# Kernel optimization log

Hardware: AMD Instinct MI355X
Metric: run time of the kernel (lower is better)

## Reference

```python
import jax, jax.numpy as jnp
import numpy as np
import math

B, L, D = 4, 4096, 1024
M = 256  # num random features
EPS = 1e-06


def setup_inputs() -> dict:
    key = jax.random.key(0)
    kq, kk, kv, kp = jax.random.split(key, 4)
    Q = jax.random.normal(kq, (B, L, D), dtype=jnp.float32)
    K = jax.random.normal(kk, (B, L, D), dtype=jnp.float32)
    V = jax.random.normal(kv, (B, L, D), dtype=jnp.float32)
    # Gaussian random projection (ortho_features=False path): shape (num_features, d_model)
    projection = jax.random.normal(kp, (M, D), dtype=jnp.float32)
    return {"Q": Q, "K": K, "V": V, "projection": projection}


def reference(Q, K, V, projection):
    d_model = Q.shape[-1]
    m = projection.shape[0]
    inv_sqrt_d = 1.0 / math.sqrt(d_model)
    # random features: exp((x / sqrt(d)) @ P^T)
    rf_q = jnp.exp(jnp.einsum('bld,md->blm', Q * inv_sqrt_d, projection)) / math.sqrt(m)  # (B,L,M)
    rf_k = jnp.exp(jnp.einsum('bld,md->blm', K * inv_sqrt_d, projection))                 # (B,L,M)
    # linear attention: KV state and normalizer
    KV = jnp.einsum('blm,bld->bmd', rf_k, V)   # (B,M,D)
    Z = jnp.sum(rf_k, axis=1)                   # (B,M)
    out = jnp.einsum('blm,bmd->bld', rf_q, KV)  # (B,L,D)
    normalizer = jnp.einsum('blm,bm->bl', rf_q, Z) + EPS  # (B,L)
    return out / normalizer[..., None]
```

## Files before the change

### kernel.cpp

```cpp
#include <hip/hip_runtime.h>
#include <math.h>

#define NB 4
#define LL 4096
#define DD 1024
#define MM 256

typedef short s16x8 __attribute__((ext_vector_type(8)));
typedef short s16x4 __attribute__((ext_vector_type(4)));
typedef float fx4 __attribute__((ext_vector_type(4)));
typedef unsigned u32x2 __attribute__((ext_vector_type(2)));
typedef unsigned u32x4 __attribute__((ext_vector_type(4)));

__device__ __forceinline__ float b2f(short s) {
  union { unsigned u; float f; } v;
  v.u = ((unsigned)(unsigned short)s) << 16;
  return v.f;
}
__device__ __forceinline__ short f2b(float f) {
  union { float f; unsigned u; } v;
  v.f = f;
  unsigned r = (v.u + 0x7fffu + ((v.u >> 16) & 1u)) >> 16;
  return (short)(unsigned short)r;
}
__device__ __forceinline__ unsigned cvt2(float lo, float hi) {
  unsigned r;
  asm("v_cvt_pk_bf16_f32 %0, %1, %2" : "=v"(r) : "v"(lo), "v"(hi));
  return r;
}
__device__ __forceinline__ int swz(int row, int col) {
  return row * 64 + (col ^ ((row & 7) << 3));
}
__device__ __forceinline__ int keyf(int m) { return (m ^ (m >> 2)) & 3; }

typedef __attribute__((address_space(1))) const void* gas1_t;
typedef __attribute__((address_space(3))) void* las3_t;
#define GLL16(g, l) __builtin_amdgcn_global_load_lds((gas1_t)(const void*)(g), (las3_t)(void*)(l), 16, 0, 0)

__global__ __launch_bounds__(256) void k_cast(const float* __restrict__ in, short* __restrict__ out, int n4) {
  int i = blockIdx.x * 256 + threadIdx.x;
  if (i >= n4) return;
  float4 v = ((const float4*)in)[i];
  s16x4 s;
  s[0] = f2b(v.x); s[1] = f2b(v.y); s[2] = f2b(v.z); s[3] = f2b(v.w);
  ((s16x4*)out)[i] = s;
}

__global__ __launch_bounds__(512, 2) void k_qk(const float* __restrict__ Q, const float* __restrict__ K,
                                               const short* __restrict__ Pb,
                                               short* __restrict__ rfq, short* __restrict__ rfkT,
                                               float* __restrict__ Zz) {
  __shared__ short As[2][8192];
  __shared__ short Bs[2][16384];
  int b = blockIdx.z;
  int l0 = blockIdx.x * 64;
  int phase = (blockIdx.x + blockIdx.z * 4) & 15;
  int tid = threadIdx.x, lane = tid & 63, w = tid >> 6;
  int wr = w >> 2, wq = w & 3;
  int m16 = lane & 15, kg = lane >> 4;

  int arow = tid >> 2, acol = (tid & 3) * 16;
  int akey = (arow & 7) << 3;
  const float* Xr = (arow < 64 ? Q + ((size_t)b * LL + l0 + arow) * DD
                               : K + ((size_t)b * LL + l0 + arow - 64) * DD) + acol;

  fx4 acc[4][4] = {};
  float4 pa[4];

  {
    int d0 = phase * 64;
    #pragma unroll
    for (int i = 0; i < 4; ++i) pa[i] = *(const float4*)(Xr + d0 + i * 4);
    #pragma unroll
    for (int j = 0; j < 4; ++j) {
      int fl = tid + j * 512, row = fl >> 3, c8 = fl & 7;
      GLL16(Pb + (size_t)row * DD + d0 + (c8 ^ (row & 7)) * 8, &Bs[0][fl * 8]);
    }
    u32x4 v0;
    v0[0] = cvt2(pa[0].x, pa[0].y); v0[1] = cvt2(pa[0].z, pa[0].w);
    v0[2] = cvt2(pa[1].x, pa[1].y); v0[3] = cvt2(pa[1].z, pa[1].w);
    *(u32x4*)&As[0][arow * 64 + (acol ^ akey)] = v0;
    v0[0] = cvt2(pa[2].x, pa[2].y); v0[1] = cvt2(pa[2].z, pa[2].w);
    v0[2] = cvt2(pa[3].x, pa[3].y); v0[3] = cvt2(pa[3].z, pa[3].w);
    *(u32x4*)&As[0][arow * 64 + ((acol + 8) ^ akey)] = v0;
  }
  __syncthreads();

  for (int t = 0; t < 16; ++t) {
    int cur = t & 1, nxt = cur ^ 1;
    if (t < 15) {
      int d1 = (((t + 1) + phase) & 15) * 64;
      #pragma unroll
      for (int i = 0; i < 4; ++i) pa[i] = *(const float4*)(Xr + d1 + i * 4);
      #pragma unroll
      for (int j = 0; j < 4; ++j) {
        int fl = tid + j * 512, row = fl >> 3, c8 = fl & 7;
        GLL16(Pb + (size_t)row * DD + d1 + (c8 ^ (row & 7)) * 8, &Bs[nxt][fl * 8]);
      }
    }
    #pragma unroll
    for (int ks = 0; ks < 2; ++ks) {
      int kb = ks * 32 + kg * 8;
      s16x8 af[4], bf[4];
      #pragma unroll
      for (int mi = 0; mi < 4; ++mi) af[mi] = *(const s16x8*)&As[cur][swz(wr * 64 + mi * 16 + m16, kb)];
      #pragma unroll
      for (int ni = 0; ni < 4; ++ni) bf[ni] = *(const s16x8*)&Bs[cur][swz(wq * 64 + ni * 16 + m16, kb)];
      #pragma unroll
      for (int mi = 0; mi < 4; ++mi)
        #pragma unroll
        for (int ni = 0; ni < 4; ++ni)
          acc[mi][ni] = __builtin_amdgcn_mfma_f32_16x16x32_bf16(af[mi], bf[ni], acc[mi][ni], 0, 0, 0);
    }
    if (t < 15) {
      u32x4 v0;
      v0[0] = cvt2(pa[0].x, pa[0].y); v0[1] = cvt2(pa[0].z, pa[0].w);
      v0[2] = cvt2(pa[1].x, pa[1].y); v0[3] = cvt2(pa[1].z, pa[1].w);
      *(u32x4*)&As[nxt][arow * 64 + (acol ^ akey)] = v0;
      v0[0] = cvt2(pa[2].x, pa[2].y); v0[1] = cvt2(pa[2].z, pa[2].w);
      v0[2] = cvt2(pa[3].x, pa[3].y); v0[3] = cvt2(pa[3].z, pa[3].w);
      *(u32x4*)&As[nxt][arow * 64 + ((acol + 8) ^ akey)] = v0;
    }
    __syncthreads();
  }

  if (wr == 0) {
    #pragma unroll
    for (int mi = 0; mi < 4; ++mi)
      #pragma unroll
      for (int ni = 0; ni < 4; ++ni) {
        int r0 = mi * 16 + (kg << 2);
        int c = wq * 64 + ni * 16 + m16;
        #pragma unroll
        for (int u = 0; u < 4; ++u)
          rfq[((size_t)b * LL + l0 + r0 + u) * MM + c] = f2b(expf(acc[mi][ni][u] * 0.03125f) * 0.0625f);
      }
  } else {
    short* T = (short*)Bs;
    float zp[4] = {0.f, 0.f, 0.f, 0.f};
    #pragma unroll
    for (int mi = 0; mi < 4; ++mi)
      #pragma unroll
      for (int ni = 0; ni < 4; ++ni) {
        int l = mi * 16 + (kg << 2);
        int m = wq * 64 + ni * 16 + m16;
        int key = (m & 7) << 3;
        float e0 = expf(acc[mi][ni][0] * 0.03125f);
        float e1 = expf(acc[mi][ni][1] * 0.03125f);
        float e2 = expf(acc[mi][ni][2] * 0.03125f);
        float e3 = expf(acc[mi][ni][3] * 0.03125f);
        zp[ni] += e0 + e1 + e2 + e3;
        *(unsigned*)&T[m * 64 + (l ^ key)] = cvt2(e0, e1);
        *(unsigned*)&T[m * 64 + ((l ^ key) + 2)] = cvt2(e2, e3);
      }
    #pragma unroll
    for (int ni = 0; ni < 4; ++ni) {
      zp[ni] += __shfl_xor(zp[ni], 16);
      zp[ni] += __shfl_xor(zp[ni], 32);
    }
    if (kg == 0) {
      #pragma unroll
      for (int ni = 0; ni < 4; ++ni)
        atomicAdd(&Zz[b * MM + wq * 64 + ni * 16 + m16], zp[ni]);
    }
  }
  __syncthreads();
  if (tid >= 256) {
    int m = tid - 256, mkey = (m & 7) << 3;
    const short* T = (const short*)Bs;
    short* dst = rfkT + ((size_t)b * MM + m) * LL + l0;
    #pragma unroll
    for (int j = 0; j < 8; ++j) {
      s16x8 v = *(const s16x8*)&T[m * 64 + ((j * 8) ^ mkey)];
      *(s16x8*)(dst + j * 8) = v;
    }
  }
}

__global__ __launch_bounds__(512) void k_kv(const float* __restrict__ V, const short* __restrict__ rfkT,
                                            float* __restrict__ KVp) {
  __shared__ float Vs[2][32 * 129];
  __shared__ short Ak[2][256 * 32];
  int d0 = blockIdx.x * 128, kc = blockIdx.y, b = blockIdx.z;
  int ls = kc * 512;
  int tid = threadIdx.x, lane = tid & 63, w = tid >> 6;
  int wm = w >> 1, wd = w & 1;
  int m16 = lane & 15, kg = lane >> 4;

  int vl = tid >> 4, vf = (tid & 15) * 8;
  const float* Vb = V + ((size_t)b * LL + ls + vl) * DD + d0 + vf;

  int am = tid >> 2, as = tid & 3;
  int acs = as ^ keyf(am);
  const short* AkS0 = rfkT + ((size_t)b * MM + am) * LL + ls + acs * 8;
  const short* AkS1 = rfkT + ((size_t)b * MM + am + 128) * LL + ls + acs * 8;

  fx4 acc[4][4] = {};
  float4 pv0, pv1;

  pv0 = *(const float4*)(Vb);
  pv1 = *(const float4*)(Vb + 4);
  GLL16(AkS0, &Ak[0][tid * 8]);
  GLL16(AkS1, &Ak[0][(tid + 512) * 8]);
  #pragma unroll
  for (int j = 0; j < 4; ++j) {
    Vs[0][vl * 129 + vf + j] = ((const float*)&pv0)[j];
    Vs[0][vl * 129 + vf + 4 + j] = ((const float*)&pv1)[j];
  }
  __syncthreads();

  for (int ch = 0; ch < 16; ++ch) {
    int cur = ch & 1, nxt = cur ^ 1;
    if (ch < 15) {
      int lo = (ch + 1) * 32;
      pv0 = *(const float4*)(Vb + (size_t)lo * DD);
      pv1 = *(const float4*)(Vb + (size_t)lo * DD + 4);
      GLL16(AkS0 + lo, &Ak[nxt][tid * 8]);
      GLL16(AkS1 + lo, &Ak[nxt][(tid + 512) * 8]);
    }
    s16x8 af[4];
    #pragma unroll
    for (int mi = 0; mi < 4; ++mi) {
      int m = wm * 64 + mi * 16 + m16;
      af[mi] = *(const s16x8*)&Ak[cur][m * 32 + ((kg ^ keyf(m)) * 8)];
    }
    #pragma unroll
    for (int ni = 0; ni < 4; ++ni) {
      int d = wd * 64 + ni * 16 + m16;
      const float* vs = &Vs[cur][kg * 8 * 129 + d];
      u32x4 bw;
      bw[0] = cvt2(vs[0], vs[129]);
      bw[1] = cvt2(vs[258], vs[387]);
      bw[2] = cvt2(vs[516], vs[645]);
      bw[3] = cvt2(vs[774], vs[903]);
      s16x8 bf = *(s16x8*)&bw;
      #pragma unroll
      for (int mi = 0; mi < 4; ++mi)
        acc[mi][ni] = __builtin_amdgcn_mfma_f32_16x16x32_bf16(af[mi], bf, acc[mi][ni], 0, 0, 0);
    }
    if (ch < 15) {
      #pragma unroll
      for (int j = 0; j < 4; ++j) {
        Vs[nxt][vl * 129 + vf + j] = ((const float*)&pv0)[j];
        Vs[nxt][vl * 129 + vf + 4 + j] = ((const float*)&pv1)[j];
      }
    }
    __syncthreads();
  }

  float* dst = KVp + (((size_t)kc * NB + b) * DD + d0) * MM;
  #pragma unroll
  for (int mi = 0; mi < 4; ++mi)
    #pragma unroll
    for (int ni = 0; ni < 4; ++ni) {
      int d = wd * 64 + ni * 16 + m16;
      int m = wm * 64 + mi * 16 + (kg << 2);
      *(float4*)(dst + (size_t)d * MM + m) = *(float4*)&acc[mi][ni];
    }
}

__global__ __launch_bounds__(256) void k_red(const float* __restrict__ KVp, short* __restrict__ KVTb) {
  int i = blockIdx.x * 256 + threadIdx.x;
  const float4* p = (const float4*)KVp;
  float4 s = p[i];
  #pragma unroll
  for (int k = 1; k < 8; ++k) {
    float4 v = p[i + k * 262144];
    s.x += v.x; s.y += v.y; s.z += v.z; s.w += v.w;
  }
  u32x2 o;
  o[0] = cvt2(s.x, s.y);
  o[1] = cvt2(s.z, s.w);
  ((u32x2*)KVTb)[i] = o;
}

__global__ __launch_bounds__(512) void k_out(const short* __restrict__ rfq, const short* __restrict__ KVTb,
                                             const float* __restrict__ Zz, float* __restrict__ out) {
  __shared__ short Aq[2][8192];
  __shared__ short Bv[2][8192];
  __shared__ float zl[256];
  __shared__ float np[512];
  __shared__ float nf[128];
  int l0 = blockIdx.x * 128, d0 = blockIdx.y * 128, b = blockIdx.z;
  int tid = threadIdx.x, lane = tid & 63, w = tid >> 6;
  int wr = w >> 2, wc = w & 3;
  const short* Ab = rfq + ((size_t)b * LL + l0) * MM;
  const short* Bb = KVTb + ((size_t)b * DD + d0) * MM;
  int f1 = tid + 512;
  int ar0 = tid >> 3, ac0 = tid & 7, ar1 = f1 >> 3, ac1 = f1 & 7;
  int nrow = tid & 127, nsub = tid >> 7;
  if (tid < 256) zl[tid] = Zz[b * MM + tid];
  fx4 acc[4][2] = {};
  float na = 0.f;

  GLL16(Ab + (size_t)ar0 * MM + (ac0 ^ (ar0 & 7)) * 8, &Aq[0][tid * 8]);
  GLL16(Ab + (size_t)ar1 * MM + (ac1 ^ (ar1 & 7)) * 8, &Aq[0][f1 * 8]);
  GLL16(Bb + (size_t)ar0 * MM + (ac0 ^ (ar0 & 7)) * 8, &Bv[0][tid * 8]);
  GLL16(Bb + (size_t)ar1 * MM + (ac1 ^ (ar1 & 7)) * 8, &Bv[0][f1 * 8]);
  __syncthreads();

  for (int t = 0; t < 4; ++t) {
    int cur = t & 1, nxt = cur ^ 1;
    if (t < 3) {
      int m1 = (t + 1) * 64;
      GLL16(Ab + (size_t)ar0 * MM + m1 + (ac0 ^ (ar0 & 7)) * 8, &Aq[nxt][tid * 8]);
      GLL16(Ab + (size_t)ar1 * MM + m1 + (ac1 ^ (ar1 & 7)) * 8, &Aq[nxt][f1 * 8]);
      GLL16(Bb + (size_t)ar0 * MM + m1 + (ac0 ^ (ar0 & 7)) * 8, &Bv[nxt][tid * 8]);
      GLL16(Bb + (size_t)ar1 * MM + m1 + (ac1 ^ (ar1 & 7)) * 8, &Bv[nxt][f1 * 8]);
    }
    #pragma unroll
    for (int kk = 0; kk < 16; ++kk) {
      int k = nsub * 16 + kk;
      na += b2f(Aq[cur][nrow * 64 + (k ^ ((nrow & 7) << 3))]) * zl[t * 64 + k];
    }
    #pragma unroll
    for (int ks = 0; ks < 2; ++ks) {
      int kb = ks * 32 + (lane >> 4) * 8;
      s16x8 af[4], bf[2];
      #pragma unroll
      for (int mi = 0; mi < 4; ++mi) {
        int row = wr * 64 + mi * 16 + (lane & 15);
        af[mi] = *(const s16x8*)&Aq[cur][row * 64 + (kb ^ ((row & 7) << 3))];
      }
      #pragma unroll
      for (int ni = 0; ni < 2; ++ni) {
        int row = wc * 32 + ni * 16 + (lane & 15);
        bf[ni] = *(const s16x8*)&Bv[cur][row * 64 + (kb ^ ((row & 7) << 3))];
      }
      #pragma unroll
      for (int mi = 0; mi < 4; ++mi)
        #pragma unroll
        for (int ni = 0; ni < 2; ++ni)
          acc[mi][ni] = __builtin_amdgcn_mfma_f32_16x16x32_bf16(af[mi], bf[ni], acc[mi][ni], 0, 0, 0);
    }
    __syncthreads();
  }
  np[tid] = na;
  __syncthreads();
  if (tid < 128) nf[tid] = np[tid] + np[tid + 128] + np[tid + 256] + np[tid + 384] + 1e-6f;
  __syncthreads();
  #pragma unroll
  for (int mi = 0; mi < 4; ++mi)
    #pragma unroll
    for (int ni = 0; ni < 2; ++ni) {
      int l = wr * 64 + mi * 16 + ((lane >> 4) << 2);
      int d = d0 + wc * 32 + ni * 16 + (lane & 15);
      #pragma unroll
      for (int u = 0; u < 4; ++u)
        out[((size_t)b * LL + l0 + l + u) * DD + d] = acc[mi][ni][u] / nf[l + u];
    }
}

extern "C" void kernel_launch(void* const* d_in, const int* in_sizes, int n_in,
                              void* d_out, int out_size, void* d_ws, size_t ws_size,
                              hipStream_t stream) {
  const float* Q = (const float*)d_in[0];
  const float* K = (const float*)d_in[1];
  const float* V = (const float*)d_in[2];
  const float* P = (const float*)d_in[3];
  float* out = (float*)d_out;
  char* ws = (char*)d_ws;

  short* Pb   = (short*)(ws + 0);
  float* Zz   = (float*)(ws + 524288);
  short* KVTb = (short*)(ws + 528384);
  short* rfq  = (short*)(ws + 4722688);
  short* rfkT = (short*)(ws + 13111296);
  float* KVp  = (float*)(ws + 21499904);

  k_cast<<<256, 256, 0, stream>>>(P, Pb, 65536);
  (void)hipMemsetAsync(Zz, 0, 4096, stream);
  k_qk<<<dim3(64, 1, NB), 512, 0, stream>>>(Q, K, Pb, rfq, rfkT, Zz);
  k_kv<<<dim3(8, 8, NB), 512, 0, stream>>>(V, rfkT, KVp);
  k_red<<<1024, 256, 0, stream>>>(KVp, KVTb);
  k_out<<<dim3(32, 8, NB), 512, 0, stream>>>(rfq, KVTb, Zz, out);
}
```

Baseline: 124.8 us.

## Fuse KV split reduction into k_kv via last-block counter and widen k_out tiles

Drops the separate k_red launch. Each k_kv block increments a per-slice atomic counter, and the last of the eight L-chunk blocks sums the partial KV slices and writes the bf16 transposed KV. k_out now covers 256 output columns per block (4x4 MFMA tiles per wave), halving the grid and the redundant rfq loads and normalizer work. k_qk also drops the per-block phase rotation of the D loop, so all blocks read the projection in the same order. The trade-offs are a serialized tail reduction in one block per slice, more LDS and registers in k_out, and possible L2 or channel hotspotting without the phase offset.

```diff
diff --git a/kernel.cpp b/kernel.cpp
--- a/kernel.cpp
+++ b/kernel.cpp
@@ -54,7 +54,6 @@
   __shared__ short Bs[2][16384];
   int b = blockIdx.z;
   int l0 = blockIdx.x * 64;
-  int phase = (blockIdx.x + blockIdx.z * 4) & 15;
   int tid = threadIdx.x, lane = tid & 63, w = tid >> 6;
   int wr = w >> 2, wq = w & 3;
   int m16 = lane & 15, kg = lane >> 4;
@@ -67,15 +66,14 @@
   fx4 acc[4][4] = {};
   float4 pa[4];
 
+  #pragma unroll
+  for (int i = 0; i < 4; ++i) pa[i] = *(const float4*)(Xr + i * 4);
+  #pragma unroll
+  for (int j = 0; j < 4; ++j) {
+    int fl = tid + j * 512, row = fl >> 3, c8 = fl & 7;
+    GLL16(Pb + (size_t)row * DD + (c8 ^ (row & 7)) * 8, &Bs[0][fl * 8]);
+  }
   {
-    int d0 = phase * 64;
-    #pragma unroll
-    for (int i = 0; i < 4; ++i) pa[i] = *(const float4*)(Xr + d0 + i * 4);
-    #pragma unroll
-    for (int j = 0; j < 4; ++j) {
-      int fl = tid + j * 512, row = fl >> 3, c8 = fl & 7;
-      GLL16(Pb + (size_t)row * DD + d0 + (c8 ^ (row & 7)) * 8, &Bs[0][fl * 8]);
-    }
     u32x4 v0;
     v0[0] = cvt2(pa[0].x, pa[0].y); v0[1] = cvt2(pa[0].z, pa[0].w);
     v0[2] = cvt2(pa[1].x, pa[1].y); v0[3] = cvt2(pa[1].z, pa[1].w);
@@ -89,7 +87,7 @@
   for (int t = 0; t < 16; ++t) {
     int cur = t & 1, nxt = cur ^ 1;
     if (t < 15) {
-      int d1 = (((t + 1) + phase) & 15) * 64;
+      int d1 = (t + 1) * 64;
       #pragma unroll
       for (int i = 0; i < 4; ++i) pa[i] = *(const float4*)(Xr + d1 + i * 4);
       #pragma unroll
@@ -178,9 +176,11 @@
 }
 
 __global__ __launch_bounds__(512) void k_kv(const float* __restrict__ V, const short* __restrict__ rfkT,
-                                            float* __restrict__ KVp) {
+                                            float* __restrict__ KVp, short* __restrict__ KVTb,
+                                            unsigned* __restrict__ cnt) {
   __shared__ float Vs[2][32 * 129];
   __shared__ short Ak[2][256 * 32];
+  __shared__ unsigned isLast;
   int d0 = blockIdx.x * 128, kc = blockIdx.y, b = blockIdx.z;
   int ls = kc * 512;
   int tid = threadIdx.x, lane = tid & 63, w = tid >> 6;
@@ -257,56 +257,76 @@
       int m = wm * 64 + mi * 16 + (kg << 2);
       *(float4*)(dst + (size_t)d * MM + m) = *(float4*)&acc[mi][ni];
     }
-}
-
-__global__ __launch_bounds__(256) void k_red(const float* __restrict__ KVp, short* __restrict__ KVTb) {
-  int i = blockIdx.x * 256 + threadIdx.x;
-  const float4* p = (const float4*)KVp;
-  float4 s = p[i];
-  #pragma unroll
-  for (int k = 1; k < 8; ++k) {
-    float4 v = p[i + k * 262144];
-    s.x += v.x; s.y += v.y; s.z += v.z; s.w += v.w;
-  }
-  u32x2 o;
-  o[0] = cvt2(s.x, s.y);
-  o[1] = cvt2(s.z, s.w);
-  ((u32x2*)KVTb)[i] = o;
+
+  __threadfence();
+  if (tid == 0) {
+    unsigned old = atomicAdd(&cnt[blockIdx.x * NB + b], 1u);
+    isLast = (old == 7u) ? 1u : 0u;
+  }
+  __syncthreads();
+  if (isLast) {
+    __threadfence();
+    const float4* p4 = (const float4*)KVp;
+    size_t sliceOff = ((size_t)b * DD + d0) * MM / 4;
+    const size_t kcStride = (size_t)NB * DD * MM / 4;
+    u32x2* o4 = (u32x2*)(KVTb + ((size_t)b * DD + d0) * MM);
+    #pragma unroll
+    for (int j = 0; j < 16; ++j) {
+      int e = tid + j * 512;
+      float4 s = p4[sliceOff + e];
+      #pragma unroll
+      for (int k = 1; k < 8; ++k) {
+        float4 v = p4[sliceOff + (size_t)k * kcStride + e];
+        s.x += v.x; s.y += v.y; s.z += v.z; s.w += v.w;
+      }
+      u32x2 o;
+      o[0] = cvt2(s.x, s.y);
+      o[1] = cvt2(s.z, s.w);
+      o4[e] = o;
+    }
+  }
 }
 
 __global__ __launch_bounds__(512) void k_out(const short* __restrict__ rfq, const short* __restrict__ KVTb,
                                              const float* __restrict__ Zz, float* __restrict__ out) {
   __shared__ short Aq[2][8192];
-  __shared__ short Bv[2][8192];
+  __shared__ short Bv[2][16384];
   __shared__ float zl[256];
   __shared__ float np[512];
   __shared__ float nf[128];
-  int l0 = blockIdx.x * 128, d0 = blockIdx.y * 128, b = blockIdx.z;
+  int l0 = blockIdx.x * 128, d0 = blockIdx.y * 256, b = blockIdx.z;
   int tid = threadIdx.x, lane = tid & 63, w = tid >> 6;
   int wr = w >> 2, wc = w & 3;
+  int m16 = lane & 15, kg = lane >> 4;
   const short* Ab = rfq + ((size_t)b * LL + l0) * MM;
   const short* Bb = KVTb + ((size_t)b * DD + d0) * MM;
-  int f1 = tid + 512;
-  int ar0 = tid >> 3, ac0 = tid & 7, ar1 = f1 >> 3, ac1 = f1 & 7;
+  int fA = tid + 512;
+  int arA = tid >> 3, acA = tid & 7, arB = fA >> 3, acB = fA & 7;
   int nrow = tid & 127, nsub = tid >> 7;
   if (tid < 256) zl[tid] = Zz[b * MM + tid];
-  fx4 acc[4][2] = {};
+  fx4 acc[4][4] = {};
   float na = 0.f;
 
-  GLL16(Ab + (size_t)ar0 * MM + (ac0 ^ (ar0 & 7)) * 8, &Aq[0][tid * 8]);
-  GLL16(Ab + (size_t)ar1 * MM + (ac1 ^ (ar1 & 7)) * 8, &Aq[0][f1 * 8]);
-  GLL16(Bb + (size_t)ar0 * MM + (ac0 ^ (ar0 & 7)) * 8, &Bv[0][tid * 8]);
-  GLL16(Bb + (size_t)ar1 * MM + (ac1 ^ (ar1 & 7)) * 8, &Bv[0][f1 * 8]);
+  GLL16(Ab + (size_t)arA * MM + (acA ^ (arA & 7)) * 8, &Aq[0][tid * 8]);
+  GLL16(Ab + (size_t)arB * MM + (acB ^ (arB & 7)) * 8, &Aq[0][fA * 8]);
+  #pragma unroll
+  for (int j = 0; j < 4; ++j) {
+    int fl = tid + j * 512, row = fl >> 3, c8 = fl & 7;
+    GLL16(Bb + (size_t)row * MM + (c8 ^ (row & 7)) * 8, &Bv[0][fl * 8]);
+  }
   __syncthreads();
 
   for (int t = 0; t < 4; ++t) {
     int cur = t & 1, nxt = cur ^ 1;
     if (t < 3) {
       int m1 = (t + 1) * 64;
-      GLL16(Ab + (size_t)ar0 * MM + m1 + (ac0 ^ (ar0 & 7)) * 8, &Aq[nxt][tid * 8]);
-      GLL16(Ab + (size_t)ar1 * MM + m1 + (ac1 ^ (ar1 & 7)) * 8, &Aq[nxt][f1 * 8]);
-      GLL16(Bb + (size_t)ar0 * MM + m1 + (ac0 ^ (ar0 & 7)) * 8, &Bv[nxt][tid * 8]);
-      GLL16(Bb + (size_t)ar1 * MM + m1 + (ac1 ^ (ar1 & 7)) * 8, &Bv[nxt][f1 * 8]);
+      GLL16(Ab + (size_t)arA * MM + m1 + (acA ^ (arA & 7)) * 8, &Aq[nxt][tid * 8]);
+      GLL16(Ab + (size_t)arB * MM + m1 + (acB ^ (arB & 7)) * 8, &Aq[nxt][fA * 8]);
+      #pragma unroll
+      for (int j = 0; j < 4; ++j) {
+        int fl = tid + j * 512, row = fl >> 3, c8 = fl & 7;
+        GLL16(Bb + (size_t)row * MM + m1 + (c8 ^ (row & 7)) * 8, &Bv[nxt][fl * 8]);
+      }
     }
     #pragma unroll
     for (int kk = 0; kk < 16; ++kk) {
@@ -315,22 +335,22 @@
     }
     #pragma unroll
     for (int ks = 0; ks < 2; ++ks) {
-      int kb = ks * 32 + (lane >> 4) * 8;
-      s16x8 af[4], bf[2];
+      int kb = ks * 32 + kg * 8;
+      s16x8 af[4], bf[4];
       #pragma unroll
       for (int mi = 0; mi < 4; ++mi) {
-        int row = wr * 64 + mi * 16 + (lane & 15);
+        int row = wr * 64 + mi * 16 + m16;
         af[mi] = *(const s16x8*)&Aq[cur][row * 64 + (kb ^ ((row & 7) << 3))];
       }
       #pragma unroll
-      for (int ni = 0; ni < 2; ++ni) {
-        int row = wc * 32 + ni * 16 + (lane & 15);
+      for (int ni = 0; ni < 4; ++ni) {
+        int row = wc * 64 + ni * 16 + m16;
         bf[ni] = *(const s16x8*)&Bv[cur][row * 64 + (kb ^ ((row & 7) << 3))];
       }
       #pragma unroll
       for (int mi = 0; mi < 4; ++mi)
         #pragma unroll
-        for (int ni = 0; ni < 2; ++ni)
+        for (int ni = 0; ni < 4; ++ni)
           acc[mi][ni] = __builtin_amdgcn_mfma_f32_16x16x32_bf16(af[mi], bf[ni], acc[mi][ni], 0, 0, 0);
     }
     __syncthreads();
@@ -342,9 +362,9 @@
   #pragma unroll
   for (int mi = 0; mi < 4; ++mi)
     #pragma unroll
-    for (int ni = 0; ni < 2; ++ni) {
-      int l = wr * 64 + mi * 16 + ((lane >> 4) << 2);
-      int d = d0 + wc * 32 + ni * 16 + (lane & 15);
+    for (int ni = 0; ni < 4; ++ni) {
+      int l = wr * 64 + mi * 16 + (kg << 2);
+      int d = d0 + wc * 64 + ni * 16 + m16;
       #pragma unroll
       for (int u = 0; u < 4; ++u)
         out[((size_t)b * LL + l0 + l + u) * DD + d] = acc[mi][ni][u] / nf[l + u];
@@ -361,17 +381,17 @@
   float* out = (float*)d_out;
   char* ws = (char*)d_ws;
 
-  short* Pb   = (short*)(ws + 0);
-  float* Zz   = (float*)(ws + 524288);
-  short* KVTb = (short*)(ws + 528384);
-  short* rfq  = (short*)(ws + 4722688);
-  short* rfkT = (short*)(ws + 13111296);
-  float* KVp  = (float*)(ws + 21499904);
+  short* Pb    = (short*)(ws + 0);
+  float* Zz    = (float*)(ws + 524288);
+  unsigned* cnt = (unsigned*)(ws + 528384);
+  short* KVTb  = (short*)(ws + 532480);
+  short* rfq   = (short*)(ws + 4722688);
+  short* rfkT  = (short*)(ws + 13111296);
+  float* KVp   = (float*)(ws + 21499904);
 
   k_cast<<<256, 256, 0, stream>>>(P, Pb, 65536);
-  (void)hipMemsetAsync(Zz, 0, 4096, stream);
+  (void)hipMemsetAsync(ws + 524288, 0, 8192, stream);
   k_qk<<<dim3(64, 1, NB), 512, 0, stream>>>(Q, K, Pb, rfq, rfkT, Zz);
-  k_kv<<<dim3(8, 8, NB), 512, 0, stream>>>(V, rfkT, KVp);
-  k_red<<<1024, 256, 0, stream>>>(KVp, KVTb);
-  k_out<<<dim3(32, 8, NB), 512, 0, stream>>>(rfq, KVTb, Zz, out);
-}
+  k_kv<<<dim3(8, 8, NB), 512, 0, stream>>>(V, rfkT, KVp, KVTb, cnt);
+  k_out<<<dim3(32, 4, NB), 512, 0, stream>>>(rfq, KVTb, Zz, out);
+}
```

Measured after the change: 201.7 us. +61.6%, slower.
